# Performance work log

Hardware: AMD Instinct MI355X
Metric: run time of the kernel (lower is better)

## Reference

```python
import jax, jax.numpy as jnp
import numpy as np

DIM = 512; HEADS = 8; DH = 64; M = 256; ITERS = 6; RK = 33; NCLS = 2

def _ln(x, g, b, eps=1e-5):
    mu = x.mean(-1, keepdims=True)
    var = ((x - mu) ** 2).mean(-1, keepdims=True)
    return (x - mu) * jax.lax.rsqrt(var + eps) * g + b

def _dwconv(x, w, b=None):
    # x: [B,C,H,W], w: [C,1,kh,kw], depthwise (groups=C)
    kh, kw = w.shape[2], w.shape[3]
    y = jax.lax.conv_general_dilated(x, w, (1, 1), [(kh // 2, kh // 2), (kw // 2, kw // 2)],
                                     feature_group_count=x.shape[1],
                                     dimension_numbers=('NCHW', 'OIHW', 'NCHW'))
    if b is not None:
        y = y + b[None, :, None, None]
    return y

def _pinv(x):
    # Moore-Penrose iterative pseudo-inverse (lucidrains nystrom-attention)
    denom = jnp.max(jnp.abs(x).sum(-1)) * jnp.max(jnp.abs(x).sum(-2))
    z = jnp.swapaxes(x, -1, -2) / denom
    I = jnp.eye(x.shape[-1], dtype=x.dtype)
    for _ in range(ITERS):
        xz = x @ z
        z = 0.25 * z @ (13 * I - xz @ (15 * I - xz @ (7 * I - xz)))
    return z

def _nystrom(x, qkv_w, out_w, out_b, res_w):
    b, n, _ = x.shape
    pad = (-n) % M  # front-pad so seq divisible by num_landmarks
    xp = jnp.pad(x, ((0, 0), (pad, 0), (0, 0)))
    q, k, v = jnp.split(xp @ qkv_w, 3, axis=-1)
    heads = lambda t: t.reshape(b, -1, HEADS, DH).transpose(0, 2, 1, 3)  # [b,h,np,d]
    q, k, v = heads(q), heads(k), heads(v)
    q = q * (DH ** -0.5)
    l = (n + pad) // M
    ql = q.reshape(b, HEADS, M, l, DH).mean(3)  # [b,h,m,d]
    kl = k.reshape(b, HEADS, M, l, DH).mean(3)
    a1 = jax.nn.softmax(jnp.einsum('bhid,bhjd->bhij', q, kl), -1)   # [b,h,np,m]
    a2 = jax.nn.softmax(jnp.einsum('bhid,bhjd->bhij', ql, kl), -1)  # [b,h,m,m]
    a3 = jax.nn.softmax(jnp.einsum('bhid,bhjd->bhij', ql, k), -1)   # [b,h,m,np]
    out = (a1 @ _pinv(a2)) @ (a3 @ v)
    # residual depthwise conv over sequence per head: v as [B,C=h,H=np,W=d]
    out = out + jax.lax.conv_general_dilated(v, res_w, (1, 1), [(RK // 2, RK // 2), (0, 0)],
                                             feature_group_count=HEADS,
                                             dimension_numbers=('NCHW', 'OIHW', 'NCHW'))
    out = out.transpose(0, 2, 1, 3).reshape(b, -1, HEADS * DH)
    return (out @ out_w + out_b)[:, -n:]

def _translayer(x, ng, nb, qkv_w, out_w, out_b, res_w):
    x = _ln(x, ng, nb)
    return x + _nystrom(x, qkv_w, out_w, out_b, res_w)

def _ppeg(x, H, W, w7, b7, w5, b5, w3, b3):
    B, _, C = x.shape
    cls, feat = x[:, 0], x[:, 1:]
    f = feat.transpose(0, 2, 1).reshape(B, C, H, W)
    y = _dwconv(f, w7, b7) + f + _dwconv(f, w5, b5) + _dwconv(f, w3, b3)
    y = y.reshape(B, C, H * W).transpose(0, 2, 1)
    return jnp.concatenate([cls[:, None], y], 1)

def setup_inputs() -> dict:
    key = jax.random.key(0)
    ks = jax.random.split(key, 20)
    B, N, F = 1, 10000, 1024
    s = 0.02
    d = {}
    d['h'] = jax.random.normal(ks[0], (B, N, F), jnp.float32)
    d['fc1_w'] = jax.random.normal(ks[1], (F, DIM)) * s
    d['fc1_b'] = jnp.zeros((DIM,))
    d['cls_token'] = jax.random.normal(ks[2], (1, 1, DIM))
    for i, p in enumerate(['l1', 'l2']):
        d[p + '_norm_g'] = jnp.ones((DIM,)); d[p + '_norm_b'] = jnp.zeros((DIM,))
        d[p + '_qkv_w'] = jax.random.normal(ks[3 + 3 * i], (DIM, 3 * DIM)) * s
        d[p + '_out_w'] = jax.random.normal(ks[4 + 3 * i], (DIM, DIM)) * s
        d[p + '_out_b'] = jnp.zeros((DIM,))
        d[p + '_res_w'] = jax.random.normal(ks[5 + 3 * i], (HEADS, 1, RK, 1)) * s
    for j, kk in enumerate([7, 5, 3]):
        d['ppeg_w%d' % kk] = jax.random.normal(ks[10 + j], (DIM, 1, kk, kk)) * s
        d['ppeg_b%d' % kk] = jnp.zeros((DIM,))
    d['norm_g'] = jnp.ones((DIM,)); d['norm_b'] = jnp.zeros((DIM,))
    d['fc2_w'] = jax.random.normal(ks[15], (DIM, NCLS)) * s
    d['fc2_b'] = jnp.zeros((NCLS,))
    return d

def reference(h, fc1_w, fc1_b, cls_token,
              l1_norm_g, l1_norm_b, l1_qkv_w, l1_out_w, l1_out_b, l1_res_w,
              ppeg_w7, ppeg_b7, ppeg_w5, ppeg_b5, ppeg_w3, ppeg_b3,
              l2_norm_g, l2_norm_b, l2_qkv_w, l2_out_w, l2_out_b, l2_res_w,
              norm_g, norm_b, fc2_w, fc2_b):
    h = jax.nn.relu(h @ fc1_w + fc1_b)
    N = h.shape[1]
    sq = int(np.ceil(np.sqrt(N)))
    add = sq * sq - N
    h = jnp.concatenate([h, h[:, :add]], 1)
    cls = jnp.broadcast_to(cls_token, (h.shape[0], 1, DIM)).astype(h.dtype)
    h = jnp.concatenate([cls, h], 1)
    h = _translayer(h, l1_norm_g, l1_norm_b, l1_qkv_w, l1_out_w, l1_out_b, l1_res_w)
    h = _ppeg(h, sq, sq, ppeg_w7, ppeg_b7, ppeg_w5, ppeg_b5, ppeg_w3, ppeg_b3)
    h = _translayer(h, l2_norm_g, l2_norm_b, l2_qkv_w, l2_out_w, l2_out_b, l2_res_w)
    h = _ln(h, norm_g, norm_b)[:, 0]
    return h @ fc2_w + fc2_b
```

## Files before the change

kernel.cpp:

```cpp
#include <hip/hip_runtime.h>
#include <math.h>

#define LPAD  10240
#define NSEQ  10001
#define PADT  239
#define NPIX  10000

typedef unsigned short u16;
typedef __attribute__((ext_vector_type(8))) short short8;
typedef __attribute__((ext_vector_type(4))) float floatx4;

__device__ __forceinline__ float b2f(u16 u){ return __uint_as_float(((unsigned)u)<<16); }
__device__ __forceinline__ u16 f2b(float f){
    unsigned x = __float_as_uint(f);
    return (u16)((x + 0x7FFFu + ((x>>16)&1u)) >> 16);
}
__device__ __forceinline__ void gld16(const void* g, void* l){
    __builtin_amdgcn_global_load_lds(
        (const __attribute__((address_space(1))) unsigned int*)g,
        (__attribute__((address_space(3))) unsigned int*)l, 16, 0, 0);
}

__global__ __launch_bounds__(256) void gemm_mfma(
    const u16* __restrict__ A, int lda, long sA,
    const u16* __restrict__ Bt, int ldb, long sB,
    void* __restrict__ Cv, int ldc, long sC,
    int M, int N, int K, int ksplit,
    const float* __restrict__ bias,
    const float* __restrict__ resid, int ldr,
    int relu, int qscale, int obf16, int atomic)
{
    __shared__ u16 As[2][64*32];
    __shared__ u16 Bs[2][128*32];

    int bz = blockIdx.z / ksplit;
    int ks = blockIdx.z - bz * ksplit;
    A  += (size_t)bz * sA;
    Bt += (size_t)bz * sB;

    int gx = gridDim.x, gy = gridDim.y;
    int nwg = gx * gy;
    int orig = blockIdx.y * gx + blockIdx.x;
    int xcd = orig & 7, lin = orig >> 3;
    int qq = nwg >> 3, rr = nwg & 7;
    int swz = (xcd < rr) ? (xcd * (qq + 1) + lin)
                         : (rr * (qq + 1) + (xcd - rr) * qq + lin);
    int bx = swz % gx, by = swz / gx;

    int kchunk = (K + ksplit - 1) / ksplit;
    kchunk = (kchunk + 31) & ~31;
    int kbeg = ks * kchunk;
    int kend = kbeg + kchunk; if (kend > K) kend = K;

    int tid = threadIdx.x;
    int w = tid >> 6, lane = tid & 63;
    int wm = (w >> 1) * 32, wn = (w & 1) * 64;
    int m0 = by * 64, n0 = bx * 128;

    int l4 = lane >> 2;
    int lk = (((lane & 3) ^ (l4 & 3)) * 8);
    int ra = w * 16 + l4;
    int rb = w * 32 + l4;
    int am0 = m0 + ra;      if (am0 > M-1) am0 = M-1;
    int bn0 = n0 + rb;      if (bn0 > N-1) bn0 = N-1;
    int bn1 = n0 + rb + 16; if (bn1 > N-1) bn1 = N-1;
    const u16* ag0 = A  + (size_t)am0 * lda + lk;
    const u16* bg0 = Bt + (size_t)bn0 * ldb + lk;
    const u16* bg1 = Bt + (size_t)bn1 * ldb + lk;
    int soA  = w * 512;
    int soB0 = w * 1024;
    int soB1 = w * 1024 + 512;

    floatx4 acc[2][4];
    #pragma unroll
    for (int i = 0; i < 2; i++)
        #pragma unroll
        for (int j = 0; j < 4; j++)
            acc[i][j] = (floatx4){0.f, 0.f, 0.f, 0.f};

    int arow = wm + (lane & 15);
    int nrow = wn + (lane & 15);
    int koff = (((lane >> 4) ^ (lane & 3)) * 8);

    if (kbeg < kend) {
        gld16(ag0 + kbeg, &As[0][soA]);
        gld16(bg0 + kbeg, &Bs[0][soB0]);
        gld16(bg1 + kbeg, &Bs[0][soB1]);
    }
    __syncthreads();

    int cb = 0;
    for (int k0 = kbeg; k0 < kend; k0 += 32) {
        int kn = k0 + 32;
        if (kn < kend) {
            gld16(ag0 + kn, &As[cb ^ 1][soA]);
            gld16(bg0 + kn, &Bs[cb ^ 1][soB0]);
            gld16(bg1 + kn, &Bs[cb ^ 1][soB1]);
        }
        short8 af[2], bf[4];
        #pragma unroll
        for (int i = 0; i < 2; i++) af[i] = *(const short8*)&As[cb][(arow + i*16)*32 + koff];
        #pragma unroll
        for (int j = 0; j < 4; j++) bf[j] = *(const short8*)&Bs[cb][(nrow + j*16)*32 + koff];
        #pragma unroll
        for (int i = 0; i < 2; i++)
            #pragma unroll
            for (int j = 0; j < 4; j++)
                acc[i][j] = __builtin_amdgcn_mfma_f32_16x16x32_bf16(af[i], bf[j], acc[i][j], 0, 0, 0);
        __syncthreads();
        cb ^= 1;
    }

    float* Cf = (float*)Cv;
    u16*   Ch = (u16*)Cv;
    size_t cb2 = (size_t)bz * sC;
    int rbase = m0 + wm + (lane >> 4) * 4;
    int cbase = n0 + wn + (lane & 15);
    #pragma unroll
    for (int i = 0; i < 2; i++) {
        #pragma unroll
        for (int j = 0; j < 4; j++) {
            int col = cbase + j * 16;
            if (col >= N) continue;
            float bcol = bias ? bias[col] : 0.f;
            #pragma unroll
            for (int r = 0; r < 4; r++) {
                int row = rbase + i * 16 + r;
                if (row >= M) continue;
                float v = acc[i][j][r];
                if (qscale && col < 512) v *= 0.125f;
                v += bcol;
                if (resid) v += resid[(size_t)row * ldr + col];
                if (relu) v = fmaxf(v, 0.f);
                size_t ci = cb2 + (size_t)row * ldc + col;
                if (obf16) Ch[ci] = f2b(v);
                else if (atomic) atomicAdd(&Cf[ci], v);
                else Cf[ci] = v;
            }
        }
    }
}

__global__ __launch_bounds__(256) void gemm_big(
    const float* __restrict__ A, int lda, long sA,
    const float* __restrict__ B, int ldb, long sB,
    float* __restrict__ C, int ldc, long sC,
    int M, int N, int K,
    float alpha, float diagc,
    const float* __restrict__ bias,
    const float* __restrict__ resid, int ldr, long sR, float rescoef,
    int btrans)
{
    __shared__ float As[2][16][20];
    __shared__ float Bs[2][16][64];

    int bz = blockIdx.z;
    A += (size_t)bz * sA;
    B += (size_t)bz * sB;
    C += (size_t)bz * sC;

    int tid = threadIdx.x;
    int tx = tid & 15, ty = tid >> 4;
    int m0 = blockIdx.y * 16, n0 = blockIdx.x * 64;

    int ar = tid >> 2;
    int ak = (tid & 3) * 4;
    int bkr = tid >> 4;
    int bc4 = (tid & 15) * 4;
    int bc  = tid >> 2;
    int bkq = (tid & 3) * 4;

    auto loadA = [&](int k0, float4& ra) {
        if (tid < 64) {
            int m = m0 + ar;
            ra = make_float4(0.f, 0.f, 0.f, 0.f);
            if (m < M) ra = *(const float4*)(A + (size_t)m * lda + k0 + ak);
        }
    };
    auto loadB = [&](int k0, float4& rb) {
        if (!btrans) rb = *(const float4*)(B + (size_t)(k0 + bkr) * ldb + n0 + bc4);
        else         rb = *(const float4*)(B + (size_t)(n0 + bc) * ldb + k0 + bkq);
    };
    auto storeA = [&](int buf, const float4& ra) {
        if (tid < 64) {
            As[buf][ak + 0][ar] = ra.x; As[buf][ak + 1][ar] = ra.y;
            As[buf][ak + 2][ar] = ra.z; As[buf][ak + 3][ar] = ra.w;
        }
    };
    auto storeB = [&](int buf, const float4& rb) {
        if (!btrans) {
            *(float4*)&Bs[buf][bkr][bc4] = rb;
        } else {
            Bs[buf][bkq + 0][bc] = rb.x; Bs[buf][bkq + 1][bc] = rb.y;
            Bs[buf][bkq + 2][bc] = rb.z; Bs[buf][bkq + 3][bc] = rb.w;
        }
    };

    float acc[4];
    #pragma unroll
    for (int j = 0; j < 4; j++) acc[j] = 0.f;

    float4 pa, pb;
    loadA(0, pa); loadB(0, pb);
    storeA(0, pa); storeB(0, pb);
    int cur = 0;

    for (int k0 = 0; k0 < K; k0 += 16) {
        bool more = (k0 + 16) < K;
        float4 na, nb;
        if (more) { loadA(k0 + 16, na); loadB(k0 + 16, nb); }
        __syncthreads();
        #pragma unroll
        for (int k = 0; k < 16; k++) {
            float a = As[cur][k][ty];
            float4 bv = *(const float4*)&Bs[cur][k][tx * 4];
            acc[0] += a * bv.x; acc[1] += a * bv.y;
            acc[2] += a * bv.z; acc[3] += a * bv.w;
        }
        if (more) { storeA(cur ^ 1, na); storeB(cur ^ 1, nb); cur ^= 1; }
    }

    int m = m0 + ty;
    if (m < M) {
        #pragma unroll
        for (int j = 0; j < 4; j++) {
            int n = n0 + tx * 4 + j;
            float v = alpha * acc[j];
            if (diagc != 0.f && m == n) v += diagc;
            if (bias) v += bias[n];
            if (resid) v += rescoef * resid[(size_t)bz * sR + (size_t)m * ldr + n];
            C[(size_t)m * ldc + n] = v;
        }
    }
}

__global__ __launch_bounds__(256, 2) void a1z_fused(
    const u16* __restrict__ QKVh, const u16* __restrict__ KLh,
    const u16* __restrict__ ZTh, float* __restrict__ OUT, int T0)
{
    __shared__ u16 Ps[64 * 264];

    int tid = threadIdx.x;
    int w = tid >> 6, lane = tid & 63;
    int lo = lane & 15, hi = lane >> 4;
    int koff = hi * 8;
    int hh = blockIdx.y;
    int tok0 = T0 + blockIdx.x * 64;

    int trow = tok0 + w * 16 + lo;
    if (trow > LPAD - 1) trow = LPAD - 1;

    const u16* qb = QKVh + (size_t)trow * 1536 + hh * 64 + koff;
    short8 aq0 = *(const short8*)(qb);
    short8 aq1 = *(const short8*)(qb + 32);

    floatx4 acc[16];
    #pragma unroll
    for (int j = 0; j < 16; j++) acc[j] = (floatx4){0.f, 0.f, 0.f, 0.f};

    const u16* klb = KLh + (size_t)hh * 256 * 64 + lo * 64 + koff;
    {
        short8 bk[16];
        #pragma unroll
        for (int j = 0; j < 16; j++) bk[j] = *(const short8*)(klb + (size_t)j * 1024);
        #pragma unroll
        for (int j = 0; j < 16; j++)
            acc[j] = __builtin_amdgcn_mfma_f32_16x16x32_bf16(aq0, bk[j], acc[j], 0, 0, 0);
    }
    {
        short8 bk[16];
        #pragma unroll
        for (int j = 0; j < 16; j++) bk[j] = *(const short8*)(klb + (size_t)j * 1024 + 32);
        #pragma unroll
        for (int j = 0; j < 16; j++)
            acc[j] = __builtin_amdgcn_mfma_f32_16x16x32_bf16(aq1, bk[j], acc[j], 0, 0, 0);
    }

    #pragma unroll
    for (int slot = 0; slot < 4; slot++) {
        float mx = acc[0][slot];
        #pragma unroll
        for (int j = 1; j < 16; j++) mx = fmaxf(mx, acc[j][slot]);
        mx = fmaxf(mx, __shfl_xor(mx, 1, 64));
        mx = fmaxf(mx, __shfl_xor(mx, 2, 64));
        mx = fmaxf(mx, __shfl_xor(mx, 4, 64));
        mx = fmaxf(mx, __shfl_xor(mx, 8, 64));
        float p[16];
        float s = 0.f;
        #pragma unroll
        for (int j = 0; j < 16; j++) { p[j] = __expf(acc[j][slot] - mx); s += p[j]; }
        s += __shfl_xor(s, 1, 64);
        s += __shfl_xor(s, 2, 64);
        s += __shfl_xor(s, 4, 64);
        s += __shfl_xor(s, 8, 64);
        float inv = 1.f / s;
        int row = w * 16 + hi * 4 + slot;
        #pragma unroll
        for (int j = 0; j < 16; j++)
            Ps[row * 264 + j * 16 + lo] = f2b(p[j] * inv);
    }

    floatx4 acc2[4];
    #pragma unroll
    for (int j = 0; j < 4; j++) acc2[j] = (floatx4){0.f, 0.f, 0.f, 0.f};
    const u16* ztb = ZTh + ((size_t)hh * 64 + lo) * 256 + koff;
    #pragma unroll
    for (int ks = 0; ks < 8; ks++) {
        short8 bz[4];
        #pragma unroll
        for (int j = 0; j < 4; j++)
            bz[j] = *(const short8*)(ztb + (size_t)j * 4096 + ks * 32);
        short8 ap = *(const short8*)&Ps[(w * 16 + lo) * 264 + ks * 32 + koff];
        #pragma unroll
        for (int j = 0; j < 4; j++)
            acc2[j] = __builtin_amdgcn_mfma_f32_16x16x32_bf16(ap, bz[j], acc2[j], 0, 0, 0);
    }
    #pragma unroll
    for (int j = 0; j < 4; j++) {
        #pragma unroll
        for (int slot = 0; slot < 4; slot++) {
            int tok = tok0 + w * 16 + hi * 4 + slot;
            if (tok < LPAD)
                OUT[(size_t)tok * 512 + hh * 64 + j * 16 + lo] = acc2[j][slot];
        }
    }
}

__global__ __launch_bounds__(256) void ln_kernel(
    const float* __restrict__ X, float* __restrict__ OUT, u16* __restrict__ OUTH,
    const float* __restrict__ g, const float* __restrict__ b, int nrows)
{
    int row = blockIdx.x * 4 + (threadIdx.x >> 6);
    int lane = threadIdx.x & 63;
    if (row >= nrows) return;
    const float* xr = X + (size_t)row * 512;
    float v[8]; float s = 0.f, s2 = 0.f;
    #pragma unroll
    for (int i = 0; i < 8; i++) { float t = xr[lane + i * 64]; v[i] = t; s += t; s2 += t * t; }
    for (int o = 1; o < 64; o <<= 1) { s += __shfl_xor(s, o, 64); s2 += __shfl_xor(s2, o, 64); }
    float mu = s * (1.f / 512.f);
    float var = s2 * (1.f / 512.f) - mu * mu;
    float rs = rsqrtf(var + 1e-5f);
    float* orow = OUT + (size_t)row * 512;
    u16* hrow = OUTH + (size_t)row * 512;
    #pragma unroll
    for (int i = 0; i < 8; i++) {
        int j = lane + i * 64;
        float y = (v[i] - mu) * rs * g[j] + b[j];
        orow[j] = y;
        hrow[j] = f2b(y);
    }
}

__global__ __launch_bounds__(64) void landmarks_kernel(
    const u16* __restrict__ QKVh, float* __restrict__ QL, float* __restrict__ KL,
    u16* __restrict__ QLh, u16* __restrict__ KLh)
{
    int mm = blockIdx.x, hh = blockIdx.y;
    int d = threadIdx.x;
    const u16* base = QKVh + (size_t)(mm * 40) * 1536 + hh * 64 + d;
    float sq = 0.f, sk = 0.f;
    for (int li = 0; li < 40; li++) {
        sq += b2f(base[(size_t)li * 1536]);
        sk += b2f(base[(size_t)li * 1536 + 512]);
    }
    size_t o = ((size_t)hh * 256 + mm) * 64 + d;
    float q = sq * (1.f / 40.f), k = sk * (1.f / 40.f);
    QL[o] = q; KL[o] = k;
    QLh[o] = f2b(q); KLh[o] = f2b(k);
}

__global__ __launch_bounds__(256) void softmax_a2(
    float* __restrict__ A2, int nrows)
{
    int row = blockIdx.x * 4 + (threadIdx.x >> 6);
    int lane = threadIdx.x & 63;
    if (row >= nrows) return;
    float* p = A2 + (size_t)row * 256 + lane * 4;
    float4 v = *(float4*)p;
    float mx = fmaxf(fmaxf(v.x, v.y), fmaxf(v.z, v.w));
    for (int o = 1; o < 64; o <<= 1) mx = fmaxf(mx, __shfl_xor(mx, o, 64));
    float4 e = make_float4(__expf(v.x - mx), __expf(v.y - mx),
                           __expf(v.z - mx), __expf(v.w - mx));
    float s = e.x + e.y + e.z + e.w;
    for (int o = 1; o < 64; o <<= 1) s += __shfl_xor(s, o, 64);
    float inv = 1.f / s;
    e.x *= inv; e.y *= inv; e.z *= inv; e.w *= inv;
    *(float4*)p = e;
}

__global__ __launch_bounds__(256) void row_softmax_bf16(
    const float* __restrict__ S, u16* __restrict__ P, int ncols)
{
    __shared__ float buf[LPAD];
    __shared__ float sr[4];
    int row = blockIdx.x;
    const float* p = S + (size_t)row * ncols;
    u16* q = P + (size_t)row * ncols;
    int tid = threadIdx.x;

    float mx = -1e30f;
    for (int i = tid * 4; i < ncols; i += 1024) {
        float4 v = *(const float4*)(p + i);
        *(float4*)&buf[i] = v;
        mx = fmaxf(mx, fmaxf(fmaxf(v.x, v.y), fmaxf(v.z, v.w)));
    }
    for (int o = 1; o < 64; o <<= 1) mx = fmaxf(mx, __shfl_xor(mx, o, 64));
    if ((tid & 63) == 0) sr[tid >> 6] = mx;
    __syncthreads();
    mx = fmaxf(fmaxf(sr[0], sr[1]), fmaxf(sr[2], sr[3]));

    float s = 0.f;
    for (int i = tid * 4; i < ncols; i += 1024) {
        float4 v = *(const float4*)&buf[i];
        s += __expf(v.x - mx) + __expf(v.y - mx) + __expf(v.z - mx) + __expf(v.w - mx);
    }
    for (int o = 1; o < 64; o <<= 1) s += __shfl_xor(s, o, 64);
    __syncthreads();
    if ((tid & 63) == 0) sr[tid >> 6] = s;
    __syncthreads();
    s = sr[0] + sr[1] + sr[2] + sr[3];
    float inv = 1.f / s;

    for (int i = tid * 4; i < ncols; i += 1024) {
        float4 v = *(const float4*)&buf[i];
        ushort4 o4;
        o4.x = f2b(__expf(v.x - mx) * inv);
        o4.y = f2b(__expf(v.y - mx) * inv);
        o4.z = f2b(__expf(v.z - mx) * inv);
        o4.w = f2b(__expf(v.w - mx) * inv);
        *(ushort4*)(q + i) = o4;
    }
}

__global__ __launch_bounds__(256) void a2norms_kernel(
    const float* __restrict__ A2, float* __restrict__ scal)
{
    int hh = blockIdx.x, tid = threadIdx.x;
    const float* A = A2 + (size_t)hh * 65536;
    float rs = 0.f, cs = 0.f;
    for (int j = 0; j < 256; j++) {
        rs += fabsf(A[(size_t)tid * 256 + j]);
        cs += fabsf(A[(size_t)j * 256 + tid]);
    }
    __shared__ float sm[8];
    for (int o = 1; o < 64; o <<= 1) {
        rs = fmaxf(rs, __shfl_xor(rs, o, 64));
        cs = fmaxf(cs, __shfl_xor(cs, o, 64));
    }
    if ((tid & 63) == 0) { sm[tid >> 6] = rs; sm[4 + (tid >> 6)] = cs; }
    __syncthreads();
    if (tid == 0) {
        float rm = fmaxf(fmaxf(sm[0], sm[1]), fmaxf(sm[2], sm[3]));
        float cm = fmaxf(fmaxf(sm[4], sm[5]), fmaxf(sm[6], sm[7]));
        atomicMax((unsigned int*)&scal[0], __float_as_uint(rm));
        atomicMax((unsigned int*)&scal[1], __float_as_uint(cm));
    }
}

__global__ __launch_bounds__(256) void z0_kernel(
    const float* __restrict__ A2, const float* __restrict__ scal,
    float* __restrict__ Zf)
{
    int i = blockIdx.x, hh = blockIdx.y, j = threadIdx.x;
    float inv = 1.f / (scal[0] * scal[1]);
    Zf[((size_t)hh * 256 + i) * 256 + j] = A2[((size_t)hh * 256 + j) * 256 + i] * inv;
}

__global__ __launch_bounds__(256) void a1z_single(
    const u16* __restrict__ QKVh, const float* __restrict__ KL,
    const float* __restrict__ ZM, float* __restrict__ OUT, int tok)
{
    int h = blockIdx.x, tid = threadIdx.x;
    __shared__ float q[64];
    __shared__ float p[256];
    __shared__ float red[4];
    if (tid < 64) q[tid] = b2f(QKVh[(size_t)tok * 1536 + h * 64 + tid]);
    __syncthreads();
    const float* kl = KL + ((size_t)h * 256 + tid) * 64;
    float s = 0.f;
    for (int d = 0; d < 64; d++) s += q[d] * kl[d];
    float mx = s;
    for (int o = 1; o < 64; o <<= 1) mx = fmaxf(mx, __shfl_xor(mx, o, 64));
    if ((tid & 63) == 0) red[tid >> 6] = mx;
    __syncthreads();
    mx = fmaxf(fmaxf(red[0], red[1]), fmaxf(red[2], red[3]));
    float e = __expf(s - mx);
    float sum = e;
    for (int o = 1; o < 64; o <<= 1) sum += __shfl_xor(sum, o, 64);
    __syncthreads();
    if ((tid & 63) == 0) red[tid >> 6] = sum;
    __syncthreads();
    sum = red[0] + red[1] + red[2] + red[3];
    p[tid] = e / sum;
    __syncthreads();
    if (tid < 64) {
        float a = 0.f;
        for (int j = 0; j < 256; j++) a += p[j] * ZM[((size_t)h * 256 + j) * 64 + tid];
        OUT[(size_t)tok * 512 + h * 64 + tid] = a;
    }
}

__global__ __launch_bounds__(256) void conv_cast(
    const u16* __restrict__ QKVh, const float* __restrict__ OUT,
    u16* __restrict__ OUTH, const float* __restrict__ resw, int T0, int ntok)
{
    __shared__ u16 Vw[48][512];
    __shared__ float ws[264];
    int tid = threadIdx.x;
    int t0 = T0 + blockIdx.x * 16;
    int wv = tid >> 6, lnn = tid & 63;
    for (int r = wv; r < 48; r += 4) {
        int ts = t0 - 16 + r;
        short8 v = (short8){0,0,0,0,0,0,0,0};
        if (ts >= 0 && ts < LPAD)
            v = *(const short8*)(QKVh + (size_t)ts * 1536 + 1024 + lnn * 8);
        *(short8*)&Vw[r][lnn * 8] = v;
    }
    if (tid < 264) ws[tid] = resw[tid];
    __syncthreads();

    int c0 = tid * 2;
    int h = c0 >> 6;
    float wreg[33];
    #pragma unroll
    for (int r = 0; r < 33; r++) wreg[r] = ws[h * 33 + r];

    #pragma unroll 1
    for (int tk = 0; tk < 16; tk++) {
        int tok = t0 + tk;
        if (tok >= T0 + ntok) break;
        float a0 = 0.f, a1 = 0.f;
        #pragma unroll
        for (int r = 0; r < 33; r++) {
            unsigned pv = *(const unsigned*)&Vw[tk + r][c0];
            a0 += wreg[r] * __uint_as_float(pv << 16);
            a1 += wreg[r] * __uint_as_float(pv & 0xFFFF0000u);
        }
        float v0 = OUT[(size_t)tok * 512 + c0]     + a0;
        float v1 = OUT[(size_t)tok * 512 + c0 + 1] + a1;
        unsigned pk = ((unsigned)f2b(v1) << 16) | (unsigned)f2b(v0);
        *(unsigned*)&OUTH[(size_t)(tok - T0) * 512 + c0] = pk;
    }
}

__global__ __launch_bounds__(256) void conv_res(
    const u16* __restrict__ QKVh, float* __restrict__ OUT,
    const float* __restrict__ resw, int t0, int ntok)
{
    int idx = blockIdx.x * 256 + threadIdx.x;
    if (idx >= ntok * 512) return;
    int tok = t0 + (idx >> 9);
    int c = idx & 511;
    int h = c >> 6;
    const u16* vbase = QKVh + 1024 + c;
    float acc = 0.f;
    #pragma unroll 1
    for (int r = 0; r < 33; r++) {
        int ts = tok - 16 + r;
        if (ts >= 0 && ts < LPAD)
            acc += resw[h * 33 + r] * b2f(vbase[(size_t)ts * 1536]);
    }
    OUT[(size_t)tok * 512 + c] += acc;
}

__global__ __launch_bounds__(256) void vtrans(
    const u16* __restrict__ QKVh, u16* __restrict__ Vt)
{
    int t0 = blockIdx.x * 64, hh = blockIdx.y;
    __shared__ u16 tile[64][65];
    #pragma unroll
    for (int ii = 0; ii < 16; ii++) {
        int idx = threadIdx.x + ii * 256;
        int t = idx >> 6, d = idx & 63;
        tile[t][d] = QKVh[(size_t)(t0 + t) * 1536 + 1024 + hh * 64 + d];
    }
    __syncthreads();
    #pragma unroll
    for (int ii = 0; ii < 16; ii++) {
        int idx = threadIdx.x + ii * 256;
        int d = idx >> 6, t = idx & 63;
        Vt[((size_t)hh * 64 + d) * LPAD + t0 + t] = tile[t][d];
    }
}

__global__ void ppeg_combine(
    const float* __restrict__ w7, const float* __restrict__ w5,
    const float* __restrict__ w3, const float* __restrict__ b7,
    const float* __restrict__ b5, const float* __restrict__ b3,
    float* __restrict__ W49, float* __restrict__ BSUM)
{
    int idx = blockIdx.x * 256 + threadIdx.x;
    if (idx >= 49 * 512) return;
    int tap = idx >> 9, c = idx & 511;
    int dy = tap / 7 - 3, dx = tap % 7 - 3;
    float v = w7[c * 49 + tap];
    if (dy >= -2 && dy <= 2 && dx >= -2 && dx <= 2)
        v += w5[c * 25 + (dy + 2) * 5 + (dx + 2)];
    if (dy >= -1 && dy <= 1 && dx >= -1 && dx <= 1)
        v += w3[c * 9 + (dy + 1) * 3 + (dx + 1)];
    W49[tap * 512 + c] = v;
    if (tap == 0) BSUM[c] = b7[c] + b5[c] + b3[c];
}

__global__ __launch_bounds__(256) void ppeg_tile(
    const float* __restrict__ S, float* __restrict__ O,
    const float* __restrict__ W49, const float* __restrict__ BSUM)
{
    __shared__ float Sw[10][22][64];
    int tid = threadIdx.x;
    int c = tid & 63;
    int sub = tid >> 6;
    int x0 = blockIdx.x * 16;
    int y0 = blockIdx.y * 4;
    int cg = blockIdx.z * 64;

    {
        int p = tid >> 4;
        int c4 = (tid & 15) * 4;
        #pragma unroll
        for (int i = 0; i < 14; i++) {
            int f = p + i * 16;
            if (f < 220) {
                int r = f / 22, xx = f - r * 22;
                int gy = y0 - 3 + r;
                int gx = x0 - 3 + xx;
                float4 v = make_float4(0.f, 0.f, 0.f, 0.f);
                if ((unsigned)gy < 100u && (unsigned)gx < 100u)
                    v = *(const float4*)(S + (size_t)(1 + gy * 100 + gx) * 512 + cg + c4);
                *(float4*)&Sw[r][xx][c4] = v;
            }
        }
    }
    float wreg[49];
    #pragma unroll
    for (int t = 0; t < 49; t++) wreg[t] = W49[t * 512 + cg + c];
    float bsum = BSUM[cg + c];
    __syncthreads();

    int xb = sub * 4;
    float acc[4][4];
    #pragma unroll
    for (int yy = 0; yy < 4; yy++)
        #pragma unroll
        for (int xq = 0; xq < 4; xq++)
            acc[yy][xq] = Sw[yy + 3][xb + xq + 3][c] + bsum;

    #pragma unroll
    for (int r = 0; r < 10; r++) {
        float v[10];
        #pragma unroll
        for (int j = 0; j < 10; j++) v[j] = Sw[r][xb + j][c];
        #pragma unroll
        for (int yy = 0; yy < 4; yy++) {
            int t = r - yy;
            if (t < 0 || t > 6) continue;
            #pragma unroll
            for (int dxt = 0; dxt < 7; dxt++) {
                float w = wreg[t * 7 + dxt];
                #pragma unroll
                for (int xq = 0; xq < 4; xq++)
                    acc[yy][xq] += v[xq + dxt] * w;
            }
        }
    }

    #pragma unroll
    for (int yy = 0; yy < 4; yy++) {
        int gy = y0 + yy;
        #pragma unroll
        for (int xq = 0; xq < 4; xq++) {
            int gx = x0 + xb + xq;
            if (gx < 100)
                O[(size_t)(1 + gy * 100 + gx) * 512 + cg + c] = acc[yy][xq];
        }
    }
}

__global__ __launch_bounds__(64) void final_kernel(
    const float* __restrict__ S, const float* __restrict__ g, const float* __restrict__ b,
    const float* __restrict__ w, const float* __restrict__ bb, float* __restrict__ out)
{
    int lane = threadIdx.x;
    float v[8]; float s = 0.f, s2 = 0.f;
    #pragma unroll
    for (int i = 0; i < 8; i++) { float t = S[lane + i * 64]; v[i] = t; s += t; s2 += t * t; }
    for (int o = 1; o < 64; o <<= 1) { s += __shfl_xor(s, o, 64); s2 += __shfl_xor(s2, o, 64); }
    float mu = s * (1.f / 512.f);
    float var = s2 * (1.f / 512.f) - mu * mu;
    float rs = rsqrtf(var + 1e-5f);
    float o0 = 0.f, o1 = 0.f;
    #pragma unroll
    for (int i = 0; i < 8; i++) {
        int j = lane + i * 64;
        float xn = (v[i] - mu) * rs * g[j] + b[j];
        o0 += xn * w[j * 2 + 0];
        o1 += xn * w[j * 2 + 1];
    }
    for (int o = 1; o < 64; o <<= 1) { o0 += __shfl_xor(o0, o, 64); o1 += __shfl_xor(o1, o, 64); }
    if (lane == 0) { out[0] = o0 + bb[0]; out[1] = o1 + bb[1]; }
}

__global__ void zerok(float* p, int n)
{
    int i = blockIdx.x * 256 + threadIdx.x;
    if (i < n) p[i] = 0.f;
}
__global__ void zero2k(float* p) { p[0] = 0.f; p[1] = 0.f; }
__global__ void copy512(float* dst, const float* src)
{
    int i = blockIdx.x * 256 + threadIdx.x;
    if (i < 512) dst[i] = src[i];
}
__global__ void cast_bf16(const float* __restrict__ src, u16* __restrict__ dst, int n)
{
    int i = (blockIdx.x * 256 + threadIdx.x) * 4;
    if (i >= n) return;
    float4 v = *(const float4*)(src + i);
    dst[i + 0] = f2b(v.x); dst[i + 1] = f2b(v.y);
    dst[i + 2] = f2b(v.z); dst[i + 3] = f2b(v.w);
}
__global__ void castT(const float* __restrict__ src, u16* __restrict__ dst,
                      int R, int C, int nb)
{
    size_t idx = (size_t)blockIdx.x * 256 + threadIdx.x;
    size_t tot = (size_t)R * C * nb;
    if (idx >= tot) return;
    int rc = R * C;
    int b = (int)(idx / rc);
    int rem = (int)(idx - (size_t)b * rc);
    int c = rem / R, r = rem - c * R;
    dst[idx] = f2b(src[(size_t)b * rc + (size_t)r * C + c]);
}

extern "C" void kernel_launch(void* const* d_in, const int* in_sizes, int n_in,
                              void* d_out, int out_size, void* d_ws, size_t ws_size,
                              hipStream_t stream)
{
    const float* h     = (const float*)d_in[0];
    const float* fc1_w = (const float*)d_in[1];
    const float* fc1_b = (const float*)d_in[2];
    const float* cls   = (const float*)d_in[3];
    bool sigorder = (in_sizes[10] == 512 * 49);
    int i_l2 = sigorder ? 16 : 10;
    int i_pp = sigorder ? 10 : 16;
    const float* l_g[2]   = { (const float*)d_in[4], (const float*)d_in[i_l2 + 0] };
    const float* l_b[2]   = { (const float*)d_in[5], (const float*)d_in[i_l2 + 1] };
    const float* l_qkv[2] = { (const float*)d_in[6], (const float*)d_in[i_l2 + 2] };
    const float* l_ow[2]  = { (const float*)d_in[7], (const float*)d_in[i_l2 + 3] };
    const float* l_ob[2]  = { (const float*)d_in[8], (const float*)d_in[i_l2 + 4] };
    const float* l_rw[2]  = { (const float*)d_in[9], (const float*)d_in[i_l2 + 5] };
    const float* w7 = (const float*)d_in[i_pp + 0];
    const float* b7 = (const float*)d_in[i_pp + 1];
    const float* w5 = (const float*)d_in[i_pp + 2];
    const float* b5 = (const float*)d_in[i_pp + 3];
    const float* w3 = (const float*)d_in[i_pp + 4];
    const float* b3 = (const float*)d_in[i_pp + 5];
    const float* ng   = (const float*)d_in[22];
    const float* nbv  = (const float*)d_in[23];
    const float* fc2w = (const float*)d_in[24];
    const float* fc2b = (const float*)d_in[25];
    float* out = (float*)d_out;

    char* Wb = (char*)d_ws;
    size_t off = 0;
    auto allocB = [&](size_t bytes) { void* p = Wb + off; off = (off + bytes + 255) & ~(size_t)255; return p; };

    float* SEQ   = (float*)allocB((size_t)NSEQ * 512 * 4);
    float* XP    = (float*)allocB((size_t)LPAD * 512 * 4);
    u16*   XPh   = (u16*)  allocB((size_t)LPAD * 512 * 2);
    u16*   QKVh  = (u16*)  allocB((size_t)LPAD * 1536 * 2);
    float* QLKL  = (float*)allocB((size_t)262144 * 4);
    float* QL = QLKL, *KL = QLKL + 131072;
    u16*   QLKLh = (u16*)  allocB((size_t)262144 * 2);
    u16*   QLh = QLKLh, *KLh = QLKLh + 131072;
    float* A2   = (float*)allocB(524288 * 4);
    float* Zf0  = (float*)allocB(524288 * 4);
    float* Zf1  = (float*)allocB(524288 * 4);
    float* XZf  = (float*)allocB(524288 * 4);
    float* W2b  = (float*)allocB(524288 * 4);
    float* W3b  = (float*)allocB(524288 * 4);
    float* A3V  = (float*)allocB(131072 * 4);
    float* ZMATf= (float*)allocB(131072 * 4);
    u16*   ZMATt= (u16*)  allocB(131072 * 2);
    u16*   Vt   = (u16*)  allocB((size_t)8 * 64 * LPAD * 2);
    u16*   fc1wt= (u16*)  allocB(524288 * 2);
    u16*   qkvwt= (u16*)  allocB(786432 * 2);
    u16*   outwt= (u16*)  allocB(262144 * 2);
    float* W49  = (float*)allocB(49 * 512 * 4);
    float* BSUM = (float*)allocB(512 * 4);
    float* SCAL = (float*)allocB(16);
    void*  U1   = allocB((size_t)LPAD * 512 * 4);
    u16*   hbf  = (u16*)U1;
    float* OUT  = (float*)U1;
    float* SEQ2 = OUT;
    size_t fixed = off;

    size_t scB_b = (size_t)8 * 256 * LPAD * 4;
    size_t phB_b = (size_t)8 * 256 * LPAD * 2;
    bool batched = ws_size >= fixed + scB_b + phB_b;
    float* SC; u16* Ph;
    if (batched) {
        SC = (float*)(Wb + fixed);
        Ph = (u16*)(Wb + fixed + scB_b);
    } else {
        SC = (float*)(Wb + fixed);
        Ph = (u16*)(Wb + fixed + (size_t)256 * LPAD * 4);
    }
    u16* OUTh = (u16*)SC;

    auto mgemm = [&](const u16* A, int lda, long sA, const u16* Bt, int ldb, long sB,
                     void* C, int ldc, long sC, int M, int N, int K,
                     const float* bias, const float* resid, int ldr,
                     int relu, int qscale, int obf16, int nbatch, int ksplit, int atomic) {
        dim3 grid((N + 127) / 128, (M + 63) / 64, nbatch * ksplit);
        gemm_mfma<<<grid, 256, 0, stream>>>(A, lda, sA, Bt, ldb, sB, C, ldc, sC,
            M, N, K, ksplit, bias, resid, ldr, relu, qscale, obf16, atomic);
    };
    auto fgemm = [&](const float* A, int lda, long sA, const float* B, int ldb, long sB,
                     float* C, int ldc, long sC, int M, int N, int K,
                     float alpha, float diagc, const float* bias,
                     const float* resid, int ldr, long sR, float rescoef,
                     int btrans, int nbatch) {
        dim3 grid(N / 64, (M + 15) / 16, nbatch);
        gemm_big<<<grid, 256, 0, stream>>>(A, lda, sA, B, ldb, sB, C, ldc, sC, M, N, K,
            alpha, diagc, bias, resid, ldr, sR, rescoef, btrans);
    };

    cast_bf16<<<(NPIX * 1024 / 4 + 255) / 256, 256, 0, stream>>>(h, hbf, NPIX * 1024);
    castT<<<(524288 + 255) / 256, 256, 0, stream>>>(fc1_w, fc1wt, 1024, 512, 1);
    mgemm(hbf, 1024, 0, fc1wt, 1024, 0, SEQ + 512, 512, 0, NPIX, 512, 1024,
          fc1_b, nullptr, 0, 1, 0, 0, 1, 1, 0);
    copy512<<<2, 256, 0, stream>>>(SEQ, cls);
    zerok<<<(PADT * 512 + 255) / 256, 256, 0, stream>>>(XP, PADT * 512);
    zerok<<<(PADT * 256 + 255) / 256, 256, 0, stream>>>((float*)XPh, PADT * 256);
    ppeg_combine<<<(49 * 512 + 255) / 256, 256, 0, stream>>>(w7, w5, w3, b7, b5, b3, W49, BSUM);

    for (int layer = 0; layer < 2; layer++) {
        const float* curSEQ = (layer == 0) ? SEQ : SEQ2;
        ln_kernel<<<(NSEQ + 3) / 4, 256, 0, stream>>>(curSEQ, XP + (size_t)PADT * 512,
            XPh + (size_t)PADT * 512, l_g[layer], l_b[layer], NSEQ);
        castT<<<(786432 + 255) / 256, 256, 0, stream>>>(l_qkv[layer], qkvwt, 512, 1536, 1);
        mgemm(XPh, 512, 0, qkvwt, 512, 0, QKVh, 1536, 0, LPAD, 1536, 512,
              nullptr, nullptr, 0, 0, 1, 1, 1, 1, 0);
        landmarks_kernel<<<dim3(256, 8), 64, 0, stream>>>(QKVh, QL, KL, QLh, KLh);
        fgemm(QL, 64, 16384, KL, 64, 16384, A2, 256, 65536, 256, 256, 64,
              1.f, 0.f, nullptr, nullptr, 0, 0, 0.f, 1, 8);
        softmax_a2<<<512, 256, 0, stream>>>(A2, 2048);
        zero2k<<<1, 1, 0, stream>>>(SCAL);
        a2norms_kernel<<<8, 256, 0, stream>>>(A2, SCAL);
        z0_kernel<<<dim3(256, 8), 256, 0, stream>>>(A2, SCAL, Zf0);

        float* zc = Zf0; float* zn = Zf1;
        for (int it = 0; it < 6; it++) {
            fgemm(A2, 256, 65536, zc, 256, 65536, XZf, 256, 65536, 256, 256, 256,
                  1.f, 0.f, nullptr, nullptr, 0, 0, 0.f, 0, 8);
            fgemm(XZf, 256, 65536, XZf, 256, 65536, W2b, 256, 65536, 256, 256, 256,
                  1.f, 15.f, nullptr, XZf, 256, 65536, -7.f, 0, 8);
            fgemm(XZf, 256, 65536, W2b, 256, 65536, W3b, 256, 65536, 256, 256, 256,
                  -1.f, 13.f, nullptr, nullptr, 0, 0, 0.f, 0, 8);
            fgemm(zc, 256, 65536, W3b, 256, 65536, zn, 256, 65536, 256, 256, 256,
                  0.25f, 0.f, nullptr, nullptr, 0, 0, 0.f, 0, 8);
            float* t = zc; zc = zn; zn = t;
        }
        float* zfin = zc;

        vtrans<<<dim3(160, 8), 256, 0, stream>>>(QKVh, Vt);
        zerok<<<512, 256, 0, stream>>>(A3V, 131072);
        if (batched) {
            mgemm(QLh, 64, 16384, QKVh + 512, 1536, 64, SC, LPAD, (long)256 * LPAD,
                  256, LPAD, 64, nullptr, nullptr, 0, 0, 0, 0, 8, 1, 0);
            row_softmax_bf16<<<2048, 256, 0, stream>>>(SC, Ph, LPAD);
            mgemm(Ph, LPAD, (long)256 * LPAD, Vt, LPAD, (long)64 * LPAD, A3V, 64, 16384,
                  256, 64, LPAD, nullptr, nullptr, 0, 0, 0, 0, 8, 40, 1);
        } else {
            for (int hh = 0; hh < 8; hh++) {
                mgemm(QLh + (size_t)hh * 16384, 64, 0, QKVh + 512 + hh * 64, 1536, 0,
                      SC, LPAD, 0, 256, LPAD, 64, nullptr, nullptr, 0, 0, 0, 0, 1, 1, 0);
                row_softmax_bf16<<<256, 256, 0, stream>>>(SC, Ph, LPAD);
                mgemm(Ph, LPAD, 0, Vt + (size_t)hh * 64 * LPAD, LPAD, 0,
                      A3V + (size_t)hh * 16384, 64, 0, 256, 64, LPAD,
                      nullptr, nullptr, 0, 0, 0, 0, 1, 40, 1);
            }
        }
        fgemm(zfin, 256, 65536, A3V, 64, 16384, ZMATf, 64, 16384, 256, 64, 256,
              1.f, 0.f, nullptr, nullptr, 0, 0, 0.f, 0, 8);

        if (layer == 0) {
            castT<<<(131072 + 255) / 256, 256, 0, stream>>>(ZMATf, ZMATt, 256, 64, 8);
            a1z_fused<<<dim3((NSEQ + 63) / 64, 8), 256, 0, stream>>>(
                QKVh, KLh, ZMATt, OUT, PADT);
            conv_cast<<<(NSEQ + 15) / 16, 256, 0, stream>>>(
                QKVh, OUT, OUTh, l_rw[0], PADT, NSEQ);
            castT<<<(262144 + 255) / 256, 256, 0, stream>>>(l_ow[0], outwt, 512, 512, 1);
            mgemm(OUTh, 512, 0, outwt, 512, 0, SEQ, 512, 0, NSEQ, 512, 512,
                  l_ob[0], XP + (size_t)PADT * 512, 512, 0, 0, 0, 1, 1, 0);
            ppeg_tile<<<dim3(7, 25, 8), 256, 0, stream>>>(SEQ, SEQ2, W49, BSUM);
            copy512<<<2, 256, 0, stream>>>(SEQ2, SEQ);
        } else {
            a1z_single<<<8, 256, 0, stream>>>(QKVh, KL, ZMATf, OUT, PADT);
            conv_res<<<2, 256, 0, stream>>>(QKVh, OUT, l_rw[1], PADT, 1);
            fgemm(OUT + (size_t)PADT * 512, 512, 0, l_ow[1], 512, 0, SEQ, 512, 0,
                  1, 512, 512, 1.f, 0.f, l_ob[1],
                  XP + (size_t)PADT * 512, 512, 0, 1.f, 0, 1);
        }
    }
    final_kernel<<<1, 64, 0, stream>>>(SEQ, ng, nbv, fc2w, fc2b, out);
    (void)n_in; (void)out_size;
}
```

Baseline: 1.518 ms.

## Drop XCD block swizzle in GEMM and retune a1z_fused register pressure

Removes the XCD-aware workgroup remapping in the MFMA GEMM and uses raw block indices for tile coordinates. In the fused a1 x pinv kernel it raises the launch-bounds occupancy hint from 2 to 3 blocks per CU. It also splits the 16-wide KL operand loads into batches of 8 to cut live registers, and double-batches the Z^T loads two k-steps at a time. This trades L2 locality across XCDs for simpler indexing, and trades some latency hiding in a1z for more resident waves.

```diff
diff --git a/kernel.cpp b/kernel.cpp
--- a/kernel.cpp
+++ b/kernel.cpp
@@ -38,15 +38,6 @@
     A  += (size_t)bz * sA;
     Bt += (size_t)bz * sB;
 
-    int gx = gridDim.x, gy = gridDim.y;
-    int nwg = gx * gy;
-    int orig = blockIdx.y * gx + blockIdx.x;
-    int xcd = orig & 7, lin = orig >> 3;
-    int qq = nwg >> 3, rr = nwg & 7;
-    int swz = (xcd < rr) ? (xcd * (qq + 1) + lin)
-                         : (rr * (qq + 1) + (xcd - rr) * qq + lin);
-    int bx = swz % gx, by = swz / gx;
-
     int kchunk = (K + ksplit - 1) / ksplit;
     kchunk = (kchunk + 31) & ~31;
     int kbeg = ks * kchunk;
@@ -55,7 +46,7 @@
     int tid = threadIdx.x;
     int w = tid >> 6, lane = tid & 63;
     int wm = (w >> 1) * 32, wn = (w & 1) * 64;
-    int m0 = by * 64, n0 = bx * 128;
+    int m0 = blockIdx.y * 64, n0 = blockIdx.x * 128;
 
     int l4 = lane >> 2;
     int lk = (((lane & 3) ^ (l4 & 3)) * 8);
@@ -234,7 +225,7 @@
     }
 }
 
-__global__ __launch_bounds__(256, 2) void a1z_fused(
+__global__ __launch_bounds__(256, 3) void a1z_fused(
     const u16* __restrict__ QKVh, const u16* __restrict__ KLh,
     const u16* __restrict__ ZTh, float* __restrict__ OUT, int T0)
 {
@@ -260,20 +251,36 @@
 
     const u16* klb = KLh + (size_t)hh * 256 * 64 + lo * 64 + koff;
     {
-        short8 bk[16];
-        #pragma unroll
-        for (int j = 0; j < 16; j++) bk[j] = *(const short8*)(klb + (size_t)j * 1024);
-        #pragma unroll
-        for (int j = 0; j < 16; j++)
+        short8 bk[8];
+        #pragma unroll
+        for (int j = 0; j < 8; j++) bk[j] = *(const short8*)(klb + (size_t)j * 1024);
+        #pragma unroll
+        for (int j = 0; j < 8; j++)
             acc[j] = __builtin_amdgcn_mfma_f32_16x16x32_bf16(aq0, bk[j], acc[j], 0, 0, 0);
     }
     {
-        short8 bk[16];
-        #pragma unroll
-        for (int j = 0; j < 16; j++) bk[j] = *(const short8*)(klb + (size_t)j * 1024 + 32);
-        #pragma unroll
-        for (int j = 0; j < 16; j++)
+        short8 bk[8];
+        #pragma unroll
+        for (int j = 0; j < 8; j++) bk[j] = *(const short8*)(klb + (size_t)(8 + j) * 1024);
+        #pragma unroll
+        for (int j = 0; j < 8; j++)
+            acc[8 + j] = __builtin_amdgcn_mfma_f32_16x16x32_bf16(aq0, bk[j], acc[8 + j], 0, 0, 0);
+    }
+    {
+        short8 bk[8];
+        #pragma unroll
+        for (int j = 0; j < 8; j++) bk[j] = *(const short8*)(klb + (size_t)j * 1024 + 32);
+        #pragma unroll
+        for (int j = 0; j < 8; j++)
             acc[j] = __builtin_amdgcn_mfma_f32_16x16x32_bf16(aq1, bk[j], acc[j], 0, 0, 0);
+    }
+    {
+        short8 bk[8];
+        #pragma unroll
+        for (int j = 0; j < 8; j++) bk[j] = *(const short8*)(klb + (size_t)(8 + j) * 1024 + 32);
+        #pragma unroll
+        for (int j = 0; j < 8; j++)
+            acc[8 + j] = __builtin_amdgcn_mfma_f32_16x16x32_bf16(aq1, bk[j], acc[8 + j], 0, 0, 0);
     }
 
     #pragma unroll
@@ -305,15 +312,22 @@
     for (int j = 0; j < 4; j++) acc2[j] = (floatx4){0.f, 0.f, 0.f, 0.f};
     const u16* ztb = ZTh + ((size_t)hh * 64 + lo) * 256 + koff;
     #pragma unroll
-    for (int ks = 0; ks < 8; ks++) {
-        short8 bz[4];
+    for (int ks = 0; ks < 8; ks += 2) {
+        short8 bz[8];
         #pragma unroll
         for (int j = 0; j < 4; j++)
             bz[j] = *(const short8*)(ztb + (size_t)j * 4096 + ks * 32);
-        short8 ap = *(const short8*)&Ps[(w * 16 + lo) * 264 + ks * 32 + koff];
         #pragma unroll
         for (int j = 0; j < 4; j++)
-            acc2[j] = __builtin_amdgcn_mfma_f32_16x16x32_bf16(ap, bz[j], acc2[j], 0, 0, 0);
+            bz[4 + j] = *(const short8*)(ztb + (size_t)j * 4096 + (ks + 1) * 32);
+        short8 ap0 = *(const short8*)&Ps[(w * 16 + lo) * 264 + ks * 32 + koff];
+        short8 ap1 = *(const short8*)&Ps[(w * 16 + lo) * 264 + (ks + 1) * 32 + koff];
+        #pragma unroll
+        for (int j = 0; j < 4; j++)
+            acc2[j] = __builtin_amdgcn_mfma_f32_16x16x32_bf16(ap0, bz[j], acc2[j], 0, 0, 0);
+        #pragma unroll
+        for (int j = 0; j < 4; j++)
+            acc2[j] = __builtin_amdgcn_mfma_f32_16x16x32_bf16(ap1, bz[4 + j], acc2[j], 0, 0, 0);
     }
     #pragma unroll
     for (int j = 0; j < 4; j++) {
```

Result: no change. 1.511 ms (-0.5%).
